# Kernel tuning notes

Hardware: AMD Instinct MI355X
Metric: run time of the kernel (lower is better)

The kernel has to match this reference:

```python
import jax, jax.numpy as jnp
import numpy as np

ALPHA = -100.0


def setup_inputs() -> dict:
    key = jax.random.key(0)
    k1, k2 = jax.random.split(key)
    input_seqs = jax.random.normal(k1, (512, 1024), dtype=jnp.float32)
    shapelets = jax.random.normal(k2, (100, 50), dtype=jnp.float32)
    return {"input_seqs": input_seqs, "shapelets": shapelets}


def reference(input_seqs, shapelets):
    """Sliding-window squared distance + softmin-weighted pooling.

    input_seqs: (n, Q) float
    shapelets : (K, L) float
    returns   : (n, K) float  -- softmin-pooled normalized sq. distance
    """
    n, Q = input_seqs.shape
    K, L = shapelets.shape
    J = Q - L  # original code uses Q - L (not Q - L + 1); kept faithful

    # ||x[j:j+L]||^2 for every window via cumulative sums (no explicit loop)
    csum = jnp.concatenate(
        [jnp.zeros((n, 1), input_seqs.dtype), jnp.cumsum(input_seqs * input_seqs, axis=1)],
        axis=1,
    )  # (n, Q+1)
    sq_win = csum[:, L:L + J] - csum[:, :J]  # (n, J)

    # cross term x[j:j+L] . s_k via windowed gather + small GEMM
    idx = jnp.arange(J)[:, None] + jnp.arange(L)[None, :]  # (J, L)
    windows = input_seqs[:, idx]  # (n, J, L)
    cross = jnp.einsum("njl,kl->njk", windows, shapelets)  # (n, J, K)

    s_sq = jnp.sum(shapelets * shapelets, axis=1)  # (K,)

    # D[i, j, k] = ||x_i[j:j+L] - s_k||^2 / L
    D = (sq_win[:, :, None] - 2.0 * cross + s_sq[None, None, :]) / L  # (n, J, K)

    # subtract per-(i,k) min over window positions (as in the original)
    Dm = D - jnp.min(D, axis=1, keepdims=True)

    # softmin-weighted average: sum_j Dm * exp(alpha*Dm) / sum_j exp(alpha*Dm)
    w = jnp.exp(ALPHA * Dm)  # stable: alpha<0 and Dm>=0 after min-shift
    M = jnp.sum(Dm * w, axis=1) / jnp.sum(w, axis=1)  # (n, K)
    return M
```

## Files before the change

### kernel.cpp

```cpp
#include <hip/hip_runtime.h>


#define N_SEQ   512
#define Q_LEN   1024
#define K_SH    100
#define L_SH    50
#define J_WIN   974
#define NTILE   7
#define MTILES  61
#define NWAVE   8
#define RINV_L  0.02f
#define PAD_SQ  4e31f
#define CQ      (-2.8853900817779268f)

#define CPR     1064
#define BLSTR   120

typedef short  short8 __attribute__((ext_vector_type(8)));
typedef float  f32x4  __attribute__((ext_vector_type(4)));
typedef unsigned int uintx4 __attribute__((ext_vector_type(4)));

union V8 { short8 s; uintx4 u; };

__device__ __forceinline__ unsigned int bf16h(float f) {
    unsigned int b = __float_as_uint(f);
    return (b + 0x7FFFu + ((b >> 16) & 1u)) >> 16;
}
__device__ __forceinline__ float bf16back(unsigned int h) {
    return __uint_as_float(h << 16);
}

__global__ __launch_bounds__(512, 2)
void softmin_mfma_kernel(const float* __restrict__ x,
                         const float* __restrict__ sh,
                         float* __restrict__ out) {
    __shared__ __align__(16) short cp[16 * CPR];
    __shared__ __align__(16) float lds_xf[1056];
    __shared__ __align__(16) float lds_sqw[984];
    __shared__ __align__(16) short bl_lds[64 * BLSTR];

    const int i    = blockIdx.x;
    const int tid  = threadIdx.x;
    const int lane = tid & 63;
    const int w    = tid >> 6;
    const int g    = lane >> 4;
    const int bcol = lane & 15;

    short8 bh[NTILE][2];
    #pragma unroll
    for (int nt = 0; nt < NTILE; ++nt) {
        const int n = nt * 16 + bcol;
        float sv[16];
        #pragma unroll
        for (int e = 0; e < 16; ++e) sv[e] = 0.f;
        if (n < K_SH) {
            const float* srow = sh + n * L_SH;
            const float2* p0 = (const float2*)(srow + 8 * g);
            #pragma unroll
            for (int q = 0; q < 4; ++q) { float2 v = p0[q]; sv[2*q] = v.x; sv[2*q+1] = v.y; }
            if (g < 2) {
                const float2* p1 = (const float2*)(srow + 32 + 8 * g);
                #pragma unroll
                for (int q = 0; q < 4; ++q) { float2 v = p1[q]; sv[8+2*q] = v.x; sv[9+2*q] = v.y; }
            } else if (g == 2) {
                float2 v = *(const float2*)(srow + 48);
                sv[8] = v.x; sv[9] = v.y;
            }
        }
        unsigned int hb[16];
        #pragma unroll
        for (int e = 0; e < 16; ++e) hb[e] = bf16h(sv[e]);
        V8 h0, h1;
        h0.u = uintx4{hb[0]|(hb[1]<<16),  hb[2]|(hb[3]<<16),  hb[4]|(hb[5]<<16),  hb[6]|(hb[7]<<16)};
        h1.u = uintx4{hb[8]|(hb[9]<<16),  hb[10]|(hb[11]<<16),hb[12]|(hb[13]<<16),hb[14]|(hb[15]<<16)};
        bh[nt][0] = h0.s; bh[nt][1] = h1.s;

        if (tid < 64) {
            unsigned int lb[16];
            #pragma unroll
            for (int e = 0; e < 16; ++e) lb[e] = bf16h(sv[e] - bf16back(hb[e]));
            *(uintx4*)&bl_lds[lane*BLSTR + nt*16] =
                uintx4{lb[0]|(lb[1]<<16),  lb[2]|(lb[3]<<16),  lb[4]|(lb[5]<<16),  lb[6]|(lb[7]<<16)};
            *(uintx4*)&bl_lds[lane*BLSTR + nt*16 + 8] =
                uintx4{lb[8]|(lb[9]<<16),  lb[10]|(lb[11]<<16),lb[12]|(lb[13]<<16),lb[14]|(lb[15]<<16)};
        }
    }

    {
        const float4* gx = (const float4*)(x + (size_t)i * Q_LEN);
        float4* lx = (float4*)lds_xf;
        if (tid < 256) lx[tid] = gx[tid];
        if (tid < 8)   lx[256 + tid] = make_float4(0.f, 0.f, 0.f, 0.f);
    }
    __syncthreads();

    if (tid < 246) {
        const float4* xf4 = (const float4*)lds_xf;
        float r0, r1, r2, r3;
        if (tid < 244) {
            float v[56];
            #pragma unroll
            for (int q = 0; q < 14; ++q) {
                float4 a = xf4[tid + q];
                v[4*q] = a.x; v[4*q+1] = a.y; v[4*q+2] = a.z; v[4*q+3] = a.w;
            }
            float s0 = 0.f;
            #pragma unroll
            for (int l = 0; l < L_SH; ++l) s0 = fmaf(v[l], v[l], s0);
            float s1 = fmaf(v[50], v[50], s0 - v[0]*v[0]);
            float s2 = fmaf(v[51], v[51], s1 - v[1]*v[1]);
            float s3 = fmaf(v[52], v[52], s2 - v[2]*v[2]);
            r0 = s0; r1 = s1; r2 = s2; r3 = s3;
            if (4*tid + 2 >= J_WIN) r2 = PAD_SQ;
            if (4*tid + 3 >= J_WIN) r3 = PAD_SQ;
        } else {
            r0 = r1 = r2 = r3 = PAD_SQ;
        }
        *(float4*)&lds_sqw[4*tid] = make_float4(r0, r1, r2, r3);
    }

    if (tid < 132) {
        const float4* xf4 = (const float4*)lds_xf;
        float4 a = xf4[2*tid], b = xf4[2*tid + 1];
        float xv[8] = {a.x, a.y, a.z, a.w, b.x, b.y, b.z, b.w};
        unsigned int hh[8], rr[8];
        #pragma unroll
        for (int e = 0; e < 8; ++e) {
            hh[e] = bf16h(xv[e]);
            rr[e] = bf16h(xv[e] - bf16back(hh[e]));
        }
        *(uintx4*)&cp[8*tid] =
            uintx4{hh[0]|(hh[1]<<16), hh[2]|(hh[3]<<16), hh[4]|(hh[5]<<16), hh[6]|(hh[7]<<16)};
        *(uintx4*)&cp[CPR + 8*tid] =
            uintx4{rr[0]|(rr[1]<<16), rr[2]|(rr[3]<<16), rr[4]|(rr[5]<<16), rr[6]|(rr[7]<<16)};
    }
    __syncthreads();

    if (tid < 262) {
        const int half = tid & 1, blk = tid >> 1;
        const uintx4 A  = *(const uintx4*)&cp[half*CPR + 8*blk];
        const uintx4 B4 = *(const uintx4*)&cp[half*CPR + 8*blk + 8];
        unsigned int s[8] = {A[0], A[1], A[2], A[3], B4[0], B4[1], B4[2], B4[3]};
        #pragma unroll
        for (int r = 1; r < 8; ++r) {
            const int p = r >> 1;
            unsigned int o[4];
            if ((r & 1) == 0) {
                #pragma unroll
                for (int e = 0; e < 4; ++e) o[e] = s[p + e];
            } else {
                #pragma unroll
                for (int e = 0; e < 4; ++e) o[e] = (s[p + e] >> 16) | (s[p + e + 1] << 16);
            }
            *(uintx4*)&cp[(2*r + half)*CPR + 8*blk] = uintx4{o[0], o[1], o[2], o[3]};
        }
    }
    __syncthreads();

    const int r7       = lane & 7;
    const int lane_off = 8 * ((lane >> 3) & 1) + 8 * g;
    const int abase0   = (2 * r7) * CPR + lane_off;

    float mreg[NTILE];
    #pragma unroll
    for (int nt = 0; nt < NTILE; ++nt) mreg[nt] = 1e30f;

    for (int mt = w; mt < MTILES; mt += NWAVE) {
        const int j0 = mt << 4;
        const int ae = abase0 + j0;
        const short8 ah0 = *(const short8*)&cp[ae];
        const short8 ah1 = *(const short8*)&cp[ae + 32];
        const float4 sqv = *(const float4*)&lds_sqw[j0 + 4 * g];

        #pragma unroll
        for (int nt = 0; nt < NTILE; ++nt) {
            f32x4 acc = {0.f, 0.f, 0.f, 0.f};
            acc = __builtin_amdgcn_mfma_f32_16x16x32_bf16(ah0, bh[nt][0], acc, 0, 0, 0);
            acc = __builtin_amdgcn_mfma_f32_16x16x32_bf16(ah1, bh[nt][1], acc, 0, 0, 0);
            const float q0 = fmaf(acc[0], -2.f, sqv.x);
            const float q1 = fmaf(acc[1], -2.f, sqv.y);
            const float q2 = fmaf(acc[2], -2.f, sqv.z);
            const float q3 = fmaf(acc[3], -2.f, sqv.w);
            mreg[nt] = fminf(mreg[nt], fminf(fminf(q0, q1), fminf(q2, q3)));
        }
    }

    float* wred = lds_xf;
    float* gm   = lds_xf + 896;
    #pragma unroll
    for (int nt = 0; nt < NTILE; ++nt) {
        float mm = mreg[nt];
        mm = fminf(mm, __shfl_xor(mm, 16));
        mm = fminf(mm, __shfl_xor(mm, 32));
        if (lane < 16) wred[(w * NTILE + nt) * 16 + lane] = mm;
    }
    __syncthreads();
    if (tid < NTILE * 16) {
        float v = wred[tid];
        #pragma unroll
        for (int ww = 1; ww < NWAVE; ++ww) v = fminf(v, wred[ww * 112 + tid]);
        gm[tid] = v;
    }
    __syncthreads();
    float mqa[NTILE];
    #pragma unroll
    for (int nt = 0; nt < NTILE; ++nt) mqa[nt] = gm[nt * 16 + bcol];

    float Sv[NTILE], Tv[NTILE], tmn[NTILE];
    #pragma unroll
    for (int nt = 0; nt < NTILE; ++nt) { Sv[nt] = 0.f; Tv[nt] = 0.f; tmn[nt] = 1e30f; }

    for (int mt = w; mt < MTILES; mt += NWAVE) {
        const int j0 = mt << 4;
        const int ae = abase0 + j0;
        const short8 ah0 = *(const short8*)&cp[ae];
        const short8 ah1 = *(const short8*)&cp[ae + 32];
        const short8 al0 = *(const short8*)&cp[ae + CPR];
        const short8 al1 = *(const short8*)&cp[ae + CPR + 32];
        const float4 sqv = *(const float4*)&lds_sqw[j0 + 4 * g];

        #pragma unroll
        for (int nt = 0; nt < NTILE; ++nt) {
            const short8 bl0 = *(const short8*)&bl_lds[lane*BLSTR + nt*16];
            const short8 bl1 = *(const short8*)&bl_lds[lane*BLSTR + nt*16 + 8];
            f32x4 acc = {0.f, 0.f, 0.f, 0.f};
            acc = __builtin_amdgcn_mfma_f32_16x16x32_bf16(ah0, bh[nt][0], acc, 0, 0, 0);
            acc = __builtin_amdgcn_mfma_f32_16x16x32_bf16(ah1, bh[nt][1], acc, 0, 0, 0);
            acc = __builtin_amdgcn_mfma_f32_16x16x32_bf16(al0, bh[nt][0], acc, 0, 0, 0);
            acc = __builtin_amdgcn_mfma_f32_16x16x32_bf16(al1, bh[nt][1], acc, 0, 0, 0);
            acc = __builtin_amdgcn_mfma_f32_16x16x32_bf16(ah0, bl0,       acc, 0, 0, 0);
            acc = __builtin_amdgcn_mfma_f32_16x16x32_bf16(ah1, bl1,       acc, 0, 0, 0);

            const float mq = mqa[nt];
            const float t0 = fmaf(acc[0], -2.f, sqv.x - mq);
            const float t1 = fmaf(acc[1], -2.f, sqv.y - mq);
            const float t2 = fmaf(acc[2], -2.f, sqv.z - mq);
            const float t3 = fmaf(acc[3], -2.f, sqv.w - mq);
            tmn[nt] = fminf(tmn[nt], fminf(fminf(t0, t1), fminf(t2, t3)));

            const float w0 = exp2f(t0 * CQ);
            const float w1 = exp2f(t1 * CQ);
            const float w2 = exp2f(t2 * CQ);
            const float w3 = exp2f(t3 * CQ);
            Sv[nt] += (w0 + w1) + (w2 + w3);
            float tv = Tv[nt];
            tv = fmaf(t0, w0, tv);
            tv = fmaf(t1, w1, tv);
            tv = fmaf(t2, w2, tv);
            tv = fmaf(t3, w3, tv);
            Tv[nt] = tv;
        }
    }

    float rm[NTILE], rS[NTILE], rT[NTILE];
    #pragma unroll
    for (int nt = 0; nt < NTILE; ++nt) {
        float a = tmn[nt], s = Sv[nt], t = Tv[nt];
        a = fminf(a, __shfl_xor(a, 16));
        a = fminf(a, __shfl_xor(a, 32));
        s += __shfl_xor(s, 16);  s += __shfl_xor(s, 32);
        t += __shfl_xor(t, 16);  t += __shfl_xor(t, 32);
        rm[nt] = a; rS[nt] = s; rT[nt] = t;
    }
    __syncthreads();
    float* redS = (float*)cp;
    float* redT = redS + 896;
    #pragma unroll
    for (int nt = 0; nt < NTILE; ++nt) {
        if (lane < 16) {
            const int idx = (w * NTILE + nt) * 16 + lane;
            wred[idx] = rm[nt];
            redS[idx] = rS[nt];
            redT[idx] = rT[nt];
        }
    }
    __syncthreads();

    if (tid < NTILE * 16) {
        float tmin = wred[tid], Sf = redS[tid], Tf = redT[tid];
        #pragma unroll
        for (int ww = 1; ww < NWAVE; ++ww) {
            tmin = fminf(tmin, wred[ww * 112 + tid]);
            Sf += redS[ww * 112 + tid];
            Tf += redT[ww * 112 + tid];
        }
        const int nt = tid >> 4, kk = tid & 15;
        const int k = nt * 16 + kk;
        if (k < K_SH) out[(size_t)i * K_SH + k] = (Tf / Sf - tmin) * RINV_L;
    }
}

extern "C" void kernel_launch(void* const* d_in, const int* in_sizes, int n_in,
                              void* d_out, int out_size, void* d_ws, size_t ws_size,
                              hipStream_t stream) {
    const float* x  = (const float*)d_in[0];
    const float* sh = (const float*)d_in[1];
    float* out = (float*)d_out;

    softmin_mfma_kernel<<<N_SEQ, 512, 0, stream>>>(x, sh, out);
}
```

Before: 102.9 us.

## Split phase-2 over shapelet tiles into two groups with dual MFMA accumulators

After: 105.3 us. +2.3%, slower.

```diff
diff --git a/kernel.cpp b/kernel.cpp
--- a/kernel.cpp
+++ b/kernel.cpp
@@ -30,6 +30,68 @@
     return __uint_as_float(h << 16);
 }
 
+#define PHASE2_GROUP(NT0, NG)                                                  \
+  {                                                                            \
+    short8 blg[NG][2];                                                         \
+    float  mqg[NG];                                                            \
+    _Pragma("unroll")                                                          \
+    for (int nn = 0; nn < NG; ++nn) {                                          \
+      blg[nn][0] = *(const short8*)&bl_lds[lane*BLSTR + (NT0+nn)*16];          \
+      blg[nn][1] = *(const short8*)&bl_lds[lane*BLSTR + (NT0+nn)*16 + 8];      \
+      mqg[nn]    = gm[(NT0+nn)*16 + bcol];                                     \
+    }                                                                          \
+    float Sg[NG], Tg[NG], tmg[NG];                                             \
+    _Pragma("unroll")                                                          \
+    for (int nn = 0; nn < NG; ++nn) { Sg[nn]=0.f; Tg[nn]=0.f; tmg[nn]=1e30f; } \
+    for (int mt = w; mt < MTILES; mt += NWAVE) {                               \
+      const int j0 = mt << 4;                                                  \
+      const int ae = abase0 + j0;                                              \
+      const short8 ah0 = *(const short8*)&cp[ae];                              \
+      const short8 ah1 = *(const short8*)&cp[ae + 32];                         \
+      const short8 al0 = *(const short8*)&cp[ae + CPR];                        \
+      const short8 al1 = *(const short8*)&cp[ae + CPR + 32];                   \
+      const float4 sqv = *(const float4*)&lds_sqw[j0 + 4*g];                   \
+      _Pragma("unroll")                                                        \
+      for (int nn = 0; nn < NG; ++nn) {                                        \
+        f32x4 a0 = {0.f,0.f,0.f,0.f}, a1 = {0.f,0.f,0.f,0.f};                  \
+        a0 = __builtin_amdgcn_mfma_f32_16x16x32_bf16(ah0, bh[NT0+nn][0], a0,0,0,0); \
+        a1 = __builtin_amdgcn_mfma_f32_16x16x32_bf16(ah1, bh[NT0+nn][1], a1,0,0,0); \
+        a0 = __builtin_amdgcn_mfma_f32_16x16x32_bf16(al0, bh[NT0+nn][0], a0,0,0,0); \
+        a1 = __builtin_amdgcn_mfma_f32_16x16x32_bf16(al1, bh[NT0+nn][1], a1,0,0,0); \
+        a0 = __builtin_amdgcn_mfma_f32_16x16x32_bf16(ah0, blg[nn][0],    a0,0,0,0); \
+        a1 = __builtin_amdgcn_mfma_f32_16x16x32_bf16(ah1, blg[nn][1],    a1,0,0,0); \
+        const float mq = mqg[nn];                                              \
+        const float t0 = fmaf(a0[0], -2.f, fmaf(a1[0], -2.f, sqv.x - mq));     \
+        const float t1 = fmaf(a0[1], -2.f, fmaf(a1[1], -2.f, sqv.y - mq));     \
+        const float t2 = fmaf(a0[2], -2.f, fmaf(a1[2], -2.f, sqv.z - mq));     \
+        const float t3 = fmaf(a0[3], -2.f, fmaf(a1[3], -2.f, sqv.w - mq));     \
+        tmg[nn] = fminf(tmg[nn], fminf(fminf(t0, t1), fminf(t2, t3)));         \
+        const float w0 = exp2f(t0 * CQ);                                       \
+        const float w1 = exp2f(t1 * CQ);                                       \
+        const float w2 = exp2f(t2 * CQ);                                       \
+        const float w3 = exp2f(t3 * CQ);                                       \
+        Sg[nn] += (w0 + w1) + (w2 + w3);                                       \
+        float tv = Tg[nn];                                                     \
+        tv = fmaf(t0, w0, tv);                                                 \
+        tv = fmaf(t1, w1, tv);                                                 \
+        tv = fmaf(t2, w2, tv);                                                 \
+        tv = fmaf(t3, w3, tv);                                                 \
+        Tg[nn] = tv;                                                           \
+      }                                                                        \
+    }                                                                          \
+    _Pragma("unroll")                                                          \
+    for (int nn = 0; nn < NG; ++nn) {                                          \
+      float a = tmg[nn], s = Sg[nn], t = Tg[nn];                               \
+      a = fminf(a, __shfl_xor(a, 16)); a = fminf(a, __shfl_xor(a, 32));        \
+      s += __shfl_xor(s, 16); s += __shfl_xor(s, 32);                          \
+      t += __shfl_xor(t, 16); t += __shfl_xor(t, 32);                          \
+      if (lane < 16) {                                                         \
+        const int idx = (w * NTILE + (NT0+nn)) * 16 + lane;                    \
+        wred[idx] = a; redS[idx] = s; redT[idx] = t;                           \
+      }                                                                        \
+    }                                                                          \
+  }
+
 __global__ __launch_bounds__(512, 2)
 void softmin_mfma_kernel(const float* __restrict__ x,
                          const float* __restrict__ sh,
@@ -38,6 +100,8 @@
     __shared__ __align__(16) float lds_xf[1056];
     __shared__ __align__(16) float lds_sqw[984];
     __shared__ __align__(16) short bl_lds[64 * BLSTR];
+    __shared__ __align__(16) float redS[NWAVE * 112];
+    __shared__ __align__(16) float redT[NWAVE * 112];
 
     const int i    = blockIdx.x;
     const int tid  = threadIdx.x;
@@ -174,13 +238,13 @@
 
         #pragma unroll
         for (int nt = 0; nt < NTILE; ++nt) {
-            f32x4 acc = {0.f, 0.f, 0.f, 0.f};
-            acc = __builtin_amdgcn_mfma_f32_16x16x32_bf16(ah0, bh[nt][0], acc, 0, 0, 0);
-            acc = __builtin_amdgcn_mfma_f32_16x16x32_bf16(ah1, bh[nt][1], acc, 0, 0, 0);
-            const float q0 = fmaf(acc[0], -2.f, sqv.x);
-            const float q1 = fmaf(acc[1], -2.f, sqv.y);
-            const float q2 = fmaf(acc[2], -2.f, sqv.z);
-            const float q3 = fmaf(acc[3], -2.f, sqv.w);
+            f32x4 a0 = {0.f, 0.f, 0.f, 0.f}, a1 = {0.f, 0.f, 0.f, 0.f};
+            a0 = __builtin_amdgcn_mfma_f32_16x16x32_bf16(ah0, bh[nt][0], a0, 0, 0, 0);
+            a1 = __builtin_amdgcn_mfma_f32_16x16x32_bf16(ah1, bh[nt][1], a1, 0, 0, 0);
+            const float q0 = fmaf(a0[0], -2.f, fmaf(a1[0], -2.f, sqv.x));
+            const float q1 = fmaf(a0[1], -2.f, fmaf(a1[1], -2.f, sqv.y));
+            const float q2 = fmaf(a0[2], -2.f, fmaf(a1[2], -2.f, sqv.z));
+            const float q3 = fmaf(a0[3], -2.f, fmaf(a1[3], -2.f, sqv.w));
             mreg[nt] = fminf(mreg[nt], fminf(fminf(q0, q1), fminf(q2, q3)));
         }
     }
@@ -202,78 +266,9 @@
         gm[tid] = v;
     }
     __syncthreads();
-    float mqa[NTILE];
-    #pragma unroll
-    for (int nt = 0; nt < NTILE; ++nt) mqa[nt] = gm[nt * 16 + bcol];
-
-    float Sv[NTILE], Tv[NTILE], tmn[NTILE];
-    #pragma unroll
-    for (int nt = 0; nt < NTILE; ++nt) { Sv[nt] = 0.f; Tv[nt] = 0.f; tmn[nt] = 1e30f; }
-
-    for (int mt = w; mt < MTILES; mt += NWAVE) {
-        const int j0 = mt << 4;
-        const int ae = abase0 + j0;
-        const short8 ah0 = *(const short8*)&cp[ae];
-        const short8 ah1 = *(const short8*)&cp[ae + 32];
-        const short8 al0 = *(const short8*)&cp[ae + CPR];
-        const short8 al1 = *(const short8*)&cp[ae + CPR + 32];
-        const float4 sqv = *(const float4*)&lds_sqw[j0 + 4 * g];
-
-        #pragma unroll
-        for (int nt = 0; nt < NTILE; ++nt) {
-            const short8 bl0 = *(const short8*)&bl_lds[lane*BLSTR + nt*16];
-            const short8 bl1 = *(const short8*)&bl_lds[lane*BLSTR + nt*16 + 8];
-            f32x4 acc = {0.f, 0.f, 0.f, 0.f};
-            acc = __builtin_amdgcn_mfma_f32_16x16x32_bf16(ah0, bh[nt][0], acc, 0, 0, 0);
-            acc = __builtin_amdgcn_mfma_f32_16x16x32_bf16(ah1, bh[nt][1], acc, 0, 0, 0);
-            acc = __builtin_amdgcn_mfma_f32_16x16x32_bf16(al0, bh[nt][0], acc, 0, 0, 0);
-            acc = __builtin_amdgcn_mfma_f32_16x16x32_bf16(al1, bh[nt][1], acc, 0, 0, 0);
-            acc = __builtin_amdgcn_mfma_f32_16x16x32_bf16(ah0, bl0,       acc, 0, 0, 0);
-            acc = __builtin_amdgcn_mfma_f32_16x16x32_bf16(ah1, bl1,       acc, 0, 0, 0);
-
-            const float mq = mqa[nt];
-            const float t0 = fmaf(acc[0], -2.f, sqv.x - mq);
-            const float t1 = fmaf(acc[1], -2.f, sqv.y - mq);
-            const float t2 = fmaf(acc[2], -2.f, sqv.z - mq);
-            const float t3 = fmaf(acc[3], -2.f, sqv.w - mq);
-            tmn[nt] = fminf(tmn[nt], fminf(fminf(t0, t1), fminf(t2, t3)));
-
-            const float w0 = exp2f(t0 * CQ);
-            const float w1 = exp2f(t1 * CQ);
-            const float w2 = exp2f(t2 * CQ);
-            const float w3 = exp2f(t3 * CQ);
-            Sv[nt] += (w0 + w1) + (w2 + w3);
-            float tv = Tv[nt];
-            tv = fmaf(t0, w0, tv);
-            tv = fmaf(t1, w1, tv);
-            tv = fmaf(t2, w2, tv);
-            tv = fmaf(t3, w3, tv);
-            Tv[nt] = tv;
-        }
-    }
-
-    float rm[NTILE], rS[NTILE], rT[NTILE];
-    #pragma unroll
-    for (int nt = 0; nt < NTILE; ++nt) {
-        float a = tmn[nt], s = Sv[nt], t = Tv[nt];
-        a = fminf(a, __shfl_xor(a, 16));
-        a = fminf(a, __shfl_xor(a, 32));
-        s += __shfl_xor(s, 16);  s += __shfl_xor(s, 32);
-        t += __shfl_xor(t, 16);  t += __shfl_xor(t, 32);
-        rm[nt] = a; rS[nt] = s; rT[nt] = t;
-    }
-    __syncthreads();
-    float* redS = (float*)cp;
-    float* redT = redS + 896;
-    #pragma unroll
-    for (int nt = 0; nt < NTILE; ++nt) {
-        if (lane < 16) {
-            const int idx = (w * NTILE + nt) * 16 + lane;
-            wred[idx] = rm[nt];
-            redS[idx] = rS[nt];
-            redT[idx] = rT[nt];
-        }
-    }
+
+    PHASE2_GROUP(0, 4)
+    PHASE2_GROUP(4, 3)
     __syncthreads();
 
     if (tid < NTILE * 16) {
```

## Partition work by shapelet tile per wave instead of by window tile

Applied to the files above, without the earlier changes.

After: 94.40 us. 8.2% less time.

```diff
diff --git a/kernel.cpp b/kernel.cpp
--- a/kernel.cpp
+++ b/kernel.cpp
@@ -8,13 +8,11 @@
 #define J_WIN   974
 #define NTILE   7
 #define MTILES  61
-#define NWAVE   8
 #define RINV_L  0.02f
 #define PAD_SQ  4e31f
 #define CQ      (-2.8853900817779268f)
 
 #define CPR     1064
-#define BLSTR   120
 
 typedef short  short8 __attribute__((ext_vector_type(8)));
 typedef float  f32x4  __attribute__((ext_vector_type(4)));
@@ -30,14 +28,13 @@
     return __uint_as_float(h << 16);
 }
 
-__global__ __launch_bounds__(512, 2)
+__global__ __launch_bounds__(448, 2)
 void softmin_mfma_kernel(const float* __restrict__ x,
                          const float* __restrict__ sh,
                          float* __restrict__ out) {
     __shared__ __align__(16) short cp[16 * CPR];
     __shared__ __align__(16) float lds_xf[1056];
     __shared__ __align__(16) float lds_sqw[984];
-    __shared__ __align__(16) short bl_lds[64 * BLSTR];
 
     const int i    = blockIdx.x;
     const int tid  = threadIdx.x;
@@ -46,10 +43,9 @@
     const int g    = lane >> 4;
     const int bcol = lane & 15;
 
-    short8 bh[NTILE][2];
-    #pragma unroll
-    for (int nt = 0; nt < NTILE; ++nt) {
-        const int n = nt * 16 + bcol;
+    short8 bh0, bh1, blo0, blo1;
+    {
+        const int n = w * 16 + bcol;
         float sv[16];
         #pragma unroll
         for (int e = 0; e < 16; ++e) sv[e] = 0.f;
@@ -67,23 +63,18 @@
                 sv[8] = v.x; sv[9] = v.y;
             }
         }
-        unsigned int hb[16];
-        #pragma unroll
-        for (int e = 0; e < 16; ++e) hb[e] = bf16h(sv[e]);
-        V8 h0, h1;
-        h0.u = uintx4{hb[0]|(hb[1]<<16),  hb[2]|(hb[3]<<16),  hb[4]|(hb[5]<<16),  hb[6]|(hb[7]<<16)};
-        h1.u = uintx4{hb[8]|(hb[9]<<16),  hb[10]|(hb[11]<<16),hb[12]|(hb[13]<<16),hb[14]|(hb[15]<<16)};
-        bh[nt][0] = h0.s; bh[nt][1] = h1.s;
-
-        if (tid < 64) {
-            unsigned int lb[16];
-            #pragma unroll
-            for (int e = 0; e < 16; ++e) lb[e] = bf16h(sv[e] - bf16back(hb[e]));
-            *(uintx4*)&bl_lds[lane*BLSTR + nt*16] =
-                uintx4{lb[0]|(lb[1]<<16),  lb[2]|(lb[3]<<16),  lb[4]|(lb[5]<<16),  lb[6]|(lb[7]<<16)};
-            *(uintx4*)&bl_lds[lane*BLSTR + nt*16 + 8] =
-                uintx4{lb[8]|(lb[9]<<16),  lb[10]|(lb[11]<<16),lb[12]|(lb[13]<<16),lb[14]|(lb[15]<<16)};
-        }
+        unsigned int hb[16], lb[16];
+        #pragma unroll
+        for (int e = 0; e < 16; ++e) {
+            hb[e] = bf16h(sv[e]);
+            lb[e] = bf16h(sv[e] - bf16back(hb[e]));
+        }
+        V8 a, b, c, d;
+        a.u = uintx4{hb[0]|(hb[1]<<16),  hb[2]|(hb[3]<<16),  hb[4]|(hb[5]<<16),  hb[6]|(hb[7]<<16)};
+        b.u = uintx4{hb[8]|(hb[9]<<16),  hb[10]|(hb[11]<<16),hb[12]|(hb[13]<<16),hb[14]|(hb[15]<<16)};
+        c.u = uintx4{lb[0]|(lb[1]<<16),  lb[2]|(lb[3]<<16),  lb[4]|(lb[5]<<16),  lb[6]|(lb[7]<<16)};
+        d.u = uintx4{lb[8]|(lb[9]<<16),  lb[10]|(lb[11]<<16),lb[12]|(lb[13]<<16),lb[14]|(lb[15]<<16)};
+        bh0 = a.s; bh1 = b.s; blo0 = c.s; blo1 = d.s;
     }
 
     {
@@ -161,56 +152,29 @@
     const int lane_off = 8 * ((lane >> 3) & 1) + 8 * g;
     const int abase0   = (2 * r7) * CPR + lane_off;
 
-    float mreg[NTILE];
-    #pragma unroll
-    for (int nt = 0; nt < NTILE; ++nt) mreg[nt] = 1e30f;
-
-    for (int mt = w; mt < MTILES; mt += NWAVE) {
+    float mreg = 1e30f;
+    for (int mt = 0; mt < MTILES; ++mt) {
         const int j0 = mt << 4;
         const int ae = abase0 + j0;
         const short8 ah0 = *(const short8*)&cp[ae];
         const short8 ah1 = *(const short8*)&cp[ae + 32];
         const float4 sqv = *(const float4*)&lds_sqw[j0 + 4 * g];
 
-        #pragma unroll
-        for (int nt = 0; nt < NTILE; ++nt) {
-            f32x4 acc = {0.f, 0.f, 0.f, 0.f};
-            acc = __builtin_amdgcn_mfma_f32_16x16x32_bf16(ah0, bh[nt][0], acc, 0, 0, 0);
-            acc = __builtin_amdgcn_mfma_f32_16x16x32_bf16(ah1, bh[nt][1], acc, 0, 0, 0);
-            const float q0 = fmaf(acc[0], -2.f, sqv.x);
-            const float q1 = fmaf(acc[1], -2.f, sqv.y);
-            const float q2 = fmaf(acc[2], -2.f, sqv.z);
-            const float q3 = fmaf(acc[3], -2.f, sqv.w);
-            mreg[nt] = fminf(mreg[nt], fminf(fminf(q0, q1), fminf(q2, q3)));
-        }
-    }
-
-    float* wred = lds_xf;
-    float* gm   = lds_xf + 896;
-    #pragma unroll
-    for (int nt = 0; nt < NTILE; ++nt) {
-        float mm = mreg[nt];
-        mm = fminf(mm, __shfl_xor(mm, 16));
-        mm = fminf(mm, __shfl_xor(mm, 32));
-        if (lane < 16) wred[(w * NTILE + nt) * 16 + lane] = mm;
-    }
-    __syncthreads();
-    if (tid < NTILE * 16) {
-        float v = wred[tid];
-        #pragma unroll
-        for (int ww = 1; ww < NWAVE; ++ww) v = fminf(v, wred[ww * 112 + tid]);
-        gm[tid] = v;
-    }
-    __syncthreads();
-    float mqa[NTILE];
-    #pragma unroll
-    for (int nt = 0; nt < NTILE; ++nt) mqa[nt] = gm[nt * 16 + bcol];
-
-    float Sv[NTILE], Tv[NTILE], tmn[NTILE];
-    #pragma unroll
-    for (int nt = 0; nt < NTILE; ++nt) { Sv[nt] = 0.f; Tv[nt] = 0.f; tmn[nt] = 1e30f; }
-
-    for (int mt = w; mt < MTILES; mt += NWAVE) {
+        f32x4 a0 = {0.f, 0.f, 0.f, 0.f}, a1 = {0.f, 0.f, 0.f, 0.f};
+        a0 = __builtin_amdgcn_mfma_f32_16x16x32_bf16(ah0, bh0, a0, 0, 0, 0);
+        a1 = __builtin_amdgcn_mfma_f32_16x16x32_bf16(ah1, bh1, a1, 0, 0, 0);
+        const float q0 = fmaf(a0[0], -2.f, fmaf(a1[0], -2.f, sqv.x));
+        const float q1 = fmaf(a0[1], -2.f, fmaf(a1[1], -2.f, sqv.y));
+        const float q2 = fmaf(a0[2], -2.f, fmaf(a1[2], -2.f, sqv.z));
+        const float q3 = fmaf(a0[3], -2.f, fmaf(a1[3], -2.f, sqv.w));
+        mreg = fminf(mreg, fminf(fminf(q0, q1), fminf(q2, q3)));
+    }
+    mreg = fminf(mreg, __shfl_xor(mreg, 16));
+    mreg = fminf(mreg, __shfl_xor(mreg, 32));
+    const float mq = mreg;
+
+    float S = 0.f, T = 0.f, tmin = 1e30f;
+    for (int mt = 0; mt < MTILES; ++mt) {
         const int j0 = mt << 4;
         const int ae = abase0 + j0;
         const short8 ah0 = *(const short8*)&cp[ae];
@@ -219,74 +183,41 @@
         const short8 al1 = *(const short8*)&cp[ae + CPR + 32];
         const float4 sqv = *(const float4*)&lds_sqw[j0 + 4 * g];
 
-        #pragma unroll
-        for (int nt = 0; nt < NTILE; ++nt) {
-            const short8 bl0 = *(const short8*)&bl_lds[lane*BLSTR + nt*16];
-            const short8 bl1 = *(const short8*)&bl_lds[lane*BLSTR + nt*16 + 8];
-            f32x4 acc = {0.f, 0.f, 0.f, 0.f};
-            acc = __builtin_amdgcn_mfma_f32_16x16x32_bf16(ah0, bh[nt][0], acc, 0, 0, 0);
-            acc = __builtin_amdgcn_mfma_f32_16x16x32_bf16(ah1, bh[nt][1], acc, 0, 0, 0);
-            acc = __builtin_amdgcn_mfma_f32_16x16x32_bf16(al0, bh[nt][0], acc, 0, 0, 0);
-            acc = __builtin_amdgcn_mfma_f32_16x16x32_bf16(al1, bh[nt][1], acc, 0, 0, 0);
-            acc = __builtin_amdgcn_mfma_f32_16x16x32_bf16(ah0, bl0,       acc, 0, 0, 0);
-            acc = __builtin_amdgcn_mfma_f32_16x16x32_bf16(ah1, bl1,       acc, 0, 0, 0);
-
-            const float mq = mqa[nt];
-            const float t0 = fmaf(acc[0], -2.f, sqv.x - mq);
-            const float t1 = fmaf(acc[1], -2.f, sqv.y - mq);
-            const float t2 = fmaf(acc[2], -2.f, sqv.z - mq);
-            const float t3 = fmaf(acc[3], -2.f, sqv.w - mq);
-            tmn[nt] = fminf(tmn[nt], fminf(fminf(t0, t1), fminf(t2, t3)));
-
-            const float w0 = exp2f(t0 * CQ);
-            const float w1 = exp2f(t1 * CQ);
-            const float w2 = exp2f(t2 * CQ);
-            const float w3 = exp2f(t3 * CQ);
-            Sv[nt] += (w0 + w1) + (w2 + w3);
-            float tv = Tv[nt];
-            tv = fmaf(t0, w0, tv);
-            tv = fmaf(t1, w1, tv);
-            tv = fmaf(t2, w2, tv);
-            tv = fmaf(t3, w3, tv);
-            Tv[nt] = tv;
-        }
-    }
-
-    float rm[NTILE], rS[NTILE], rT[NTILE];
-    #pragma unroll
-    for (int nt = 0; nt < NTILE; ++nt) {
-        float a = tmn[nt], s = Sv[nt], t = Tv[nt];
-        a = fminf(a, __shfl_xor(a, 16));
-        a = fminf(a, __shfl_xor(a, 32));
-        s += __shfl_xor(s, 16);  s += __shfl_xor(s, 32);
-        t += __shfl_xor(t, 16);  t += __shfl_xor(t, 32);
-        rm[nt] = a; rS[nt] = s; rT[nt] = t;
-    }
-    __syncthreads();
-    float* redS = (float*)cp;
-    float* redT = redS + 896;
-    #pragma unroll
-    for (int nt = 0; nt < NTILE; ++nt) {
-        if (lane < 16) {
-            const int idx = (w * NTILE + nt) * 16 + lane;
-            wred[idx] = rm[nt];
-            redS[idx] = rS[nt];
-            redT[idx] = rT[nt];
-        }
-    }
-    __syncthreads();
-
-    if (tid < NTILE * 16) {
-        float tmin = wred[tid], Sf = redS[tid], Tf = redT[tid];
-        #pragma unroll
-        for (int ww = 1; ww < NWAVE; ++ww) {
-            tmin = fminf(tmin, wred[ww * 112 + tid]);
-            Sf += redS[ww * 112 + tid];
-            Tf += redT[ww * 112 + tid];
-        }
-        const int nt = tid >> 4, kk = tid & 15;
-        const int k = nt * 16 + kk;
-        if (k < K_SH) out[(size_t)i * K_SH + k] = (Tf / Sf - tmin) * RINV_L;
+        f32x4 a0 = {0.f, 0.f, 0.f, 0.f}, a1 = {0.f, 0.f, 0.f, 0.f};
+        a0 = __builtin_amdgcn_mfma_f32_16x16x32_bf16(ah0, bh0,  a0, 0, 0, 0);
+        a1 = __builtin_amdgcn_mfma_f32_16x16x32_bf16(ah1, bh1,  a1, 0, 0, 0);
+        a0 = __builtin_amdgcn_mfma_f32_16x16x32_bf16(al0, bh0,  a0, 0, 0, 0);
+        a1 = __builtin_amdgcn_mfma_f32_16x16x32_bf16(al1, bh1,  a1, 0, 0, 0);
+        a0 = __builtin_amdgcn_mfma_f32_16x16x32_bf16(ah0, blo0, a0, 0, 0, 0);
+        a1 = __builtin_amdgcn_mfma_f32_16x16x32_bf16(ah1, blo1, a1, 0, 0, 0);
+
+        const float t0 = fmaf(a0[0], -2.f, fmaf(a1[0], -2.f, sqv.x - mq));
+        const float t1 = fmaf(a0[1], -2.f, fmaf(a1[1], -2.f, sqv.y - mq));
+        const float t2 = fmaf(a0[2], -2.f, fmaf(a1[2], -2.f, sqv.z - mq));
+        const float t3 = fmaf(a0[3], -2.f, fmaf(a1[3], -2.f, sqv.w - mq));
+        tmin = fminf(tmin, fminf(fminf(t0, t1), fminf(t2, t3)));
+
+        const float w0 = exp2f(t0 * CQ);
+        const float w1 = exp2f(t1 * CQ);
+        const float w2 = exp2f(t2 * CQ);
+        const float w3 = exp2f(t3 * CQ);
+        S += (w0 + w1) + (w2 + w3);
+        float tv = T;
+        tv = fmaf(t0, w0, tv);
+        tv = fmaf(t1, w1, tv);
+        tv = fmaf(t2, w2, tv);
+        tv = fmaf(t3, w3, tv);
+        T = tv;
+    }
+
+    tmin = fminf(tmin, __shfl_xor(tmin, 16));
+    tmin = fminf(tmin, __shfl_xor(tmin, 32));
+    S += __shfl_xor(S, 16);  S += __shfl_xor(S, 32);
+    T += __shfl_xor(T, 16);  T += __shfl_xor(T, 32);
+
+    if (lane < 16) {
+        const int k = w * 16 + lane;
+        if (k < K_SH) out[(size_t)i * K_SH + k] = (T / S - tmin) * RINV_L;
     }
 }
 
@@ -297,5 +228,5 @@
     const float* sh = (const float*)d_in[1];
     float* out = (float*)d_out;
 
-    softmin_mfma_kernel<<<N_SEQ, 512, 0, stream>>>(x, sh, out);
-}
+    softmin_mfma_kernel<<<N_SEQ, 448, 0, stream>>>(x, sh, out);
+}
```
